# Performance work log

Measured on AMD Instinct MI355X. Metric: run time of the kernel, lower is better.

The kernel has to match this reference:

```python
import jax, jax.numpy as jnp
import numpy as np

N_WIRES = 8
DIM = 2 ** N_WIRES  # 256
NUM_HEADS = 4

def _cnot_ring_perm():
    # Compose CNOT(w, w+1) for w=0..6 then CNOT(7, 0) into one basis permutation.
    # Wire 0 is the most-significant bit of the basis index.
    perm = np.arange(DIM)
    pairs = [(w, w + 1) for w in range(N_WIRES - 1)] + [(N_WIRES - 1, 0)]
    j = np.arange(DIM)
    for c, t in pairs:
        ctrl = (j >> (N_WIRES - 1 - c)) & 1
        M = j ^ (ctrl << (N_WIRES - 1 - t))  # flip target bit where control=1 (involution)
        perm = perm[M]
    return perm

PERM = _cnot_ring_perm()
# SIGNS[i, w] = <i|Z_w|i> = 1 - 2*bit_w(i)
SIGNS = np.array([[1.0 - 2.0 * ((i >> (N_WIRES - 1 - w)) & 1) for w in range(N_WIRES)]
                  for i in range(DIM)], dtype=np.float32)

def setup_inputs() -> dict:
    key = jax.random.key(0)
    k1, k2, k3 = jax.random.split(key, 3)
    x = jax.random.normal(k1, (16, 4096, N_WIRES), jnp.float32)  # rotation angles per token
    theta = jax.random.normal(k2, (N_WIRES,), jnp.float32)       # trainable RX params
    w_combine = jax.random.normal(k3, (N_WIRES, N_WIRES), jnp.float32) / np.float32(np.sqrt(N_WIRES))
    b_combine = jnp.zeros((N_WIRES,), jnp.float32)
    return {"x": x, "theta": theta, "w_combine": w_combine, "b_combine": b_combine}

def _quantum_features(x, theta):
    # RX(x_i) then RX(theta_i) on wire i compose to RX(x_i + theta_i) acting on |0>.
    B, S, E = x.shape
    N = B * S
    phi = (x + theta).reshape(N, E)
    c = jnp.cos(0.5 * phi).astype(jnp.complex64)
    s = (-1j) * jnp.sin(0.5 * phi)          # RX|0> = cos(phi/2)|0> - i sin(phi/2)|1>
    wv = jnp.stack([c, s.astype(jnp.complex64)], axis=-1)  # (N, 8, 2)
    # Build product state via successive Kronecker products (wire 0 = MSB).
    state = jnp.ones((N, 1), jnp.complex64)
    for w in range(E):
        state = (state[:, :, None] * wv[:, w, None, :]).reshape(N, -1)  # (N, 2^(w+1))
    state = state[:, jnp.asarray(PERM)]      # apply the CNOT ring as one permutation
    probs = state.real ** 2 + state.imag ** 2  # (N, 256)
    return (probs @ jnp.asarray(SIGNS)).reshape(B, S, E)  # <Z_w> per token

def reference(x, theta, w_combine, b_combine):
    B, S, E = x.shape
    d_k = E // NUM_HEADS
    q = _quantum_features(x, theta)           # (B, S, 8); k = v = q in the source
    scores = jnp.einsum('bse,bte->bst', q, q) / np.float32(np.sqrt(d_k))
    attn = jax.nn.softmax(scores, axis=-1)    # dropout is identity in eval mode
    out = jnp.einsum('bst,bte->bse', attn, q)
    # Faithful to source: transpose(1,2).contiguous().view(B, S, E)
    out = jnp.swapaxes(out, 1, 2).reshape(B, S, E)
    return out @ w_combine.T + b_combine
```

## Files before the change

### kernel.cpp

```cpp
#include <hip/hip_runtime.h>
#include <math.h>


#define SEQ   4096
#define NB    16
#define SROWS 128
#define TPB   1024
#define NTG   4
#define TC    1024
#define NCH   (SEQ / TC)
#define TILES_PER_TG 8
#define KSTR  12
#define VSTR  1028

typedef _Float16 f16x4  __attribute__((ext_vector_type(4)));
typedef float    f32x16 __attribute__((ext_vector_type(16)));
typedef __fp16   hf2    __attribute__((ext_vector_type(2)));

#if __has_builtin(__builtin_amdgcn_exp2f)
#define EXP2F(x) __builtin_amdgcn_exp2f(x)
#else
#define EXP2F(x) exp2f(x)
#endif

__global__ __launch_bounds__(TPB, 8)
void qattn_kernel(const float* __restrict__ x, const float* __restrict__ theta,
                  const float* __restrict__ wc, const float* __restrict__ bc,
                  float* __restrict__ out)
{
    __shared__ __align__(16) _Float16 kf[TC * KSTR];
    __shared__ __align__(16) _Float16 vt[9 * VSTR];
    float* part = (float*)kf;
    float* attn = (float*)vt;

    const int tid  = threadIdx.x;
    const int lane = tid & 63;
    const int wv   = tid >> 6;
    const int sub  = wv & 3;
    const int tg   = wv >> 2;
    const int l31  = lane & 31;
    const int hp   = lane >> 5;

    const int b  = blockIdx.x >> 5;
    const int S0 = (blockIdx.x & 31) * SROWS;
    const float* xb = x + (size_t)b * SEQ * 8;

    float th[8];
#pragma unroll
    for (int w = 0; w < 8; ++w) th[w] = theta[w];

    vt[8 * VSTR + tid] = (_Float16)1.0f;

    f16x4 qfrag;
    {
        const int s = S0 + sub * 32 + l31;
        const float4 xa  = *(const float4*)(xb + s * 8);
        const float4 xb4 = *(const float4*)(xb + s * 8 + 4);
        float c0 = __cosf(xa.x  + th[0]);
        float c1 = __cosf(xa.y  + th[1]);
        float c2 = __cosf(xa.z  + th[2]);
        float c3 = __cosf(xa.w  + th[3]);
        float c4 = __cosf(xb4.x + th[4]);
        float c5 = __cosf(xb4.y + th[5]);
        float c6 = __cosf(xb4.z + th[6]);
        float c7 = __cosf(xb4.w + th[7]);
        float p1 = c0 * c1, p2 = p1 * c2, p3 = p2 * c3, p4 = p3 * c4;
        float p5 = p4 * c5, p6 = p5 * c6, p7 = p6 * c7;
        float p0 = c1 * c2 * c3 * c4 * c5 * c6 * c7;
        const float sc = 0.70710678118654752f * 1.44269504088896341f;
        if (hp == 0)
            qfrag = (f16x4){(_Float16)(p0*sc), (_Float16)(p1*sc),
                            (_Float16)(p2*sc), (_Float16)(p3*sc)};
        else
            qfrag = (f16x4){(_Float16)(p4*sc), (_Float16)(p5*sc),
                            (_Float16)(p6*sc), (_Float16)(p7*sc)};
    }

    f32x16 o = {0.f,0.f,0.f,0.f,0.f,0.f,0.f,0.f,0.f,0.f,0.f,0.f,0.f,0.f,0.f,0.f};

    const int wr = (l31 < 8) ? l31 : 8;
    const _Float16* kfb = kf + l31 * KSTR + 4 * hp + (tg * TILES_PER_TG) * 32 * KSTR;
    const _Float16* vbb = vt + wr * VSTR + 4 * hp + tg * (TILES_PER_TG * 32);

    float4 pxa = *(const float4*)(xb + tid * 8);
    float4 pxb = *(const float4*)(xb + tid * 8 + 4);

    for (int ch = 0; ch < NCH; ++ch) {
        float c0 = __cosf(pxa.x + th[0]);
        float c1 = __cosf(pxa.y + th[1]);
        float c2 = __cosf(pxa.z + th[2]);
        float c3 = __cosf(pxa.w + th[3]);
        float c4 = __cosf(pxb.x + th[4]);
        float c5 = __cosf(pxb.y + th[5]);
        float c6 = __cosf(pxb.z + th[6]);
        float c7 = __cosf(pxb.w + th[7]);
        float p1 = c0 * c1, p2 = p1 * c2, p3 = p2 * c3, p4 = p3 * c4;
        float p5 = p4 * c5, p6 = p5 * c6, p7 = p6 * c7;
        float p0 = c1 * c2 * c3 * c4 * c5 * c6 * c7;
        _Float16 h0 = (_Float16)p0, h1 = (_Float16)p1, h2 = (_Float16)p2,
                 h3 = (_Float16)p3, h4 = (_Float16)p4, h5 = (_Float16)p5,
                 h6 = (_Float16)p6, h7 = (_Float16)p7;
        __syncthreads();
        {
            _Float16* krow = kf + tid * KSTR;
            *(f16x4*)(krow)     = (f16x4){h0, h1, h2, h3};
            *(f16x4*)(krow + 4) = (f16x4){h4, h5, h6, h7};
            vt[0 * VSTR + tid] = h0;
            vt[1 * VSTR + tid] = h1;
            vt[2 * VSTR + tid] = h2;
            vt[3 * VSTR + tid] = h3;
            vt[4 * VSTR + tid] = h4;
            vt[5 * VSTR + tid] = h5;
            vt[6 * VSTR + tid] = h6;
            vt[7 * VSTR + tid] = h7;
        }
        __syncthreads();
        {
            const int nt = ((ch + 1 < NCH) ? (ch + 1) * TC : ch * TC) + tid;
            pxa = *(const float4*)(xb + nt * 8);
            pxb = *(const float4*)(xb + nt * 8 + 4);
        }
#pragma unroll 4
        for (int i = 0; i < TILES_PER_TG; ++i) {
            f16x4 kfrag = *(const f16x4*)(kfb + i * 32 * KSTR);
            f32x16 cc = __builtin_amdgcn_mfma_f32_32x32x8f16(
                kfrag, qfrag, (f32x16){0.f,0.f,0.f,0.f,0.f,0.f,0.f,0.f,
                                       0.f,0.f,0.f,0.f,0.f,0.f,0.f,0.f}, 0, 0, 0);
#pragma unroll
            for (int u = 0; u < 4; ++u) {
                union { hf2 h[2]; f16x4 v; } pu;
                pu.h[0] = __builtin_amdgcn_cvt_pkrtz(EXP2F(cc[4*u+0]), EXP2F(cc[4*u+1]));
                pu.h[1] = __builtin_amdgcn_cvt_pkrtz(EXP2F(cc[4*u+2]), EXP2F(cc[4*u+3]));
                f16x4 vfrag = *(const f16x4*)(vbb + i * 32 + u * 8);
                o = __builtin_amdgcn_mfma_f32_32x32x8f16(pu.v, vfrag, o, 0, 0, 0);
            }
        }
    }

    __syncthreads();
    if (l31 < 9) {
#pragma unroll
        for (int r = 0; r < 16; ++r) {
            const int sloc = sub * 32 + (r & 3) + 8 * (r >> 2) + 4 * hp;
            part[((tg * SROWS) + sloc) * 9 + l31] = o[r];
        }
    }
    __syncthreads();
    for (int idx = tid; idx < SROWS * 9; idx += TPB) {
        const int rr = idx / 9;
        const int w  = idx - rr * 9;
        float sm = 0.f;
#pragma unroll
        for (int g = 0; g < NTG; ++g) sm += part[((g * SROWS) + rr) * 9 + w];
        attn[rr * 9 + w] = sm;
    }
    __syncthreads();
    if (tid < SROWS * 8) {
        const int rr = tid >> 3;
        const int w  = tid & 7;
        attn[rr * 9 + w] = attn[rr * 9 + w] / attn[rr * 9 + 8];
    }
    __syncthreads();

    if (tid < SROWS) {
        const int e    = tid >> 4;
        const int nloc = tid & 15;
        const int r    = e * 512 + (S0 >> 3) + nloc;
        float y[8];
#pragma unroll
        for (int c = 0; c < 8; ++c) y[c] = attn[(nloc * 8 + c) * 9 + e];
        float oo[8];
#pragma unroll
        for (int k = 0; k < 8; ++k) {
            float a = bc[k];
#pragma unroll
            for (int c = 0; c < 8; ++c) a += y[c] * wc[k * 8 + c];
            oo[k] = a;
        }
        float4* op = (float4*)(out + ((size_t)b * SEQ + r) * 8);
        op[0] = make_float4(oo[0], oo[1], oo[2], oo[3]);
        op[1] = make_float4(oo[4], oo[5], oo[6], oo[7]);
    }
}

extern "C" void kernel_launch(void* const* d_in, const int* in_sizes, int n_in,
                              void* d_out, int out_size, void* d_ws, size_t ws_size,
                              hipStream_t stream)
{
    const float* x  = (const float*)d_in[0];
    const float* th = (const float*)d_in[1];
    const float* wc = (const float*)d_in[2];
    const float* bc = (const float*)d_in[3];
    float* out = (float*)d_out;

    qattn_kernel<<<dim3(NB * (SEQ / SROWS)), dim3(TPB), 0, stream>>>(x, th, wc, bc, out);
}
```

Before: 90.86 us.

## Switch attention MFMAs to 32x32x16 f16 with lane-shuffled P fragments

Replaces the 32x32x8 f16 MFMAs with the gfx950 32x32x16 variant. The score MFMA now runs once per tile with K zero-padded from 8 to 16, and the PV product uses two K=16 MFMAs instead of four K=8 ones, with the exp'd probabilities rearranged across half-waves through xor-32 shuffles. This is meant to halve the matrix instruction count in the inner loop, at the cost of extra cross-lane shuffles, selects and a wider K stride. It also drops the register prefetch of the next chunk's x and loads it inside the barrier region instead, which may expose global load latency.

```diff
diff --git a/kernel.cpp b/kernel.cpp
--- a/kernel.cpp
+++ b/kernel.cpp
@@ -10,10 +10,11 @@
 #define TC    1024
 #define NCH   (SEQ / TC)
 #define TILES_PER_TG 8
-#define KSTR  12
+#define KSTR  20
 #define VSTR  1028
 
 typedef _Float16 f16x4  __attribute__((ext_vector_type(4)));
+typedef _Float16 f16x8  __attribute__((ext_vector_type(8)));
 typedef float    f32x16 __attribute__((ext_vector_type(16)));
 typedef __fp16   hf2    __attribute__((ext_vector_type(2)));
 
@@ -49,9 +50,15 @@
 #pragma unroll
     for (int w = 0; w < 8; ++w) th[w] = theta[w];
 
-    vt[8 * VSTR + tid] = (_Float16)1.0f;
-
-    f16x4 qfrag;
+    {
+        f16x4 z = {(_Float16)0.f, (_Float16)0.f, (_Float16)0.f, (_Float16)0.f};
+        *(f16x4*)(kf + tid * KSTR + 8)  = z;
+        *(f16x4*)(kf + tid * KSTR + 12) = z;
+        vt[8 * VSTR + tid] = (_Float16)1.0f;
+    }
+
+    f16x8 qfrag = {(_Float16)0.f, (_Float16)0.f, (_Float16)0.f, (_Float16)0.f,
+                   (_Float16)0.f, (_Float16)0.f, (_Float16)0.f, (_Float16)0.f};
     {
         const int s = S0 + sub * 32 + l31;
         const float4 xa  = *(const float4*)(xb + s * 8);
@@ -69,39 +76,40 @@
         float p0 = c1 * c2 * c3 * c4 * c5 * c6 * c7;
         const float sc = 0.70710678118654752f * 1.44269504088896341f;
         if (hp == 0)
-            qfrag = (f16x4){(_Float16)(p0*sc), (_Float16)(p1*sc),
-                            (_Float16)(p2*sc), (_Float16)(p3*sc)};
-        else
-            qfrag = (f16x4){(_Float16)(p4*sc), (_Float16)(p5*sc),
+            qfrag = (f16x8){(_Float16)(p0*sc), (_Float16)(p1*sc),
+                            (_Float16)(p2*sc), (_Float16)(p3*sc),
+                            (_Float16)(p4*sc), (_Float16)(p5*sc),
                             (_Float16)(p6*sc), (_Float16)(p7*sc)};
     }
 
-    f32x16 o = {0.f,0.f,0.f,0.f,0.f,0.f,0.f,0.f,0.f,0.f,0.f,0.f,0.f,0.f,0.f,0.f};
+    const f32x16 Z = {0.f,0.f,0.f,0.f,0.f,0.f,0.f,0.f,
+                      0.f,0.f,0.f,0.f,0.f,0.f,0.f,0.f};
+    f32x16 o = Z;
 
     const int wr = (l31 < 8) ? l31 : 8;
-    const _Float16* kfb = kf + l31 * KSTR + 4 * hp + (tg * TILES_PER_TG) * 32 * KSTR;
-    const _Float16* vbb = vt + wr * VSTR + 4 * hp + tg * (TILES_PER_TG * 32);
-
-    float4 pxa = *(const float4*)(xb + tid * 8);
-    float4 pxb = *(const float4*)(xb + tid * 8 + 4);
+    const _Float16* kfb = kf + l31 * KSTR + 8 * hp + (tg * TILES_PER_TG) * 32 * KSTR;
+    const _Float16* vbb = vt + wr * VSTR + 8 * hp + tg * (TILES_PER_TG * 32);
 
     for (int ch = 0; ch < NCH; ++ch) {
-        float c0 = __cosf(pxa.x + th[0]);
-        float c1 = __cosf(pxa.y + th[1]);
-        float c2 = __cosf(pxa.z + th[2]);
-        float c3 = __cosf(pxa.w + th[3]);
-        float c4 = __cosf(pxb.x + th[4]);
-        float c5 = __cosf(pxb.y + th[5]);
-        float c6 = __cosf(pxb.z + th[6]);
-        float c7 = __cosf(pxb.w + th[7]);
-        float p1 = c0 * c1, p2 = p1 * c2, p3 = p2 * c3, p4 = p3 * c4;
-        float p5 = p4 * c5, p6 = p5 * c6, p7 = p6 * c7;
-        float p0 = c1 * c2 * c3 * c4 * c5 * c6 * c7;
-        _Float16 h0 = (_Float16)p0, h1 = (_Float16)p1, h2 = (_Float16)p2,
-                 h3 = (_Float16)p3, h4 = (_Float16)p4, h5 = (_Float16)p5,
-                 h6 = (_Float16)p6, h7 = (_Float16)p7;
         __syncthreads();
         {
+            const int t = ch * TC + tid;
+            const float4 xa  = *(const float4*)(xb + t * 8);
+            const float4 xb4 = *(const float4*)(xb + t * 8 + 4);
+            float c0 = __cosf(xa.x  + th[0]);
+            float c1 = __cosf(xa.y  + th[1]);
+            float c2 = __cosf(xa.z  + th[2]);
+            float c3 = __cosf(xa.w  + th[3]);
+            float c4 = __cosf(xb4.x + th[4]);
+            float c5 = __cosf(xb4.y + th[5]);
+            float c6 = __cosf(xb4.z + th[6]);
+            float c7 = __cosf(xb4.w + th[7]);
+            float p1 = c0 * c1, p2 = p1 * c2, p3 = p2 * c3, p4 = p3 * c4;
+            float p5 = p4 * c5, p6 = p5 * c6, p7 = p6 * c7;
+            float p0 = c1 * c2 * c3 * c4 * c5 * c6 * c7;
+            _Float16 h0 = (_Float16)p0, h1 = (_Float16)p1, h2 = (_Float16)p2,
+                     h3 = (_Float16)p3, h4 = (_Float16)p4, h5 = (_Float16)p5,
+                     h6 = (_Float16)p6, h7 = (_Float16)p7;
             _Float16* krow = kf + tid * KSTR;
             *(f16x4*)(krow)     = (f16x4){h0, h1, h2, h3};
             *(f16x4*)(krow + 4) = (f16x4){h4, h5, h6, h7};
@@ -115,25 +123,45 @@
             vt[7 * VSTR + tid] = h7;
         }
         __syncthreads();
-        {
-            const int nt = ((ch + 1 < NCH) ? (ch + 1) * TC : ch * TC) + tid;
-            pxa = *(const float4*)(xb + nt * 8);
-            pxb = *(const float4*)(xb + nt * 8 + 4);
-        }
-#pragma unroll 4
+#pragma unroll 2
         for (int i = 0; i < TILES_PER_TG; ++i) {
-            f16x4 kfrag = *(const f16x4*)(kfb + i * 32 * KSTR);
-            f32x16 cc = __builtin_amdgcn_mfma_f32_32x32x8f16(
-                kfrag, qfrag, (f32x16){0.f,0.f,0.f,0.f,0.f,0.f,0.f,0.f,
-                                       0.f,0.f,0.f,0.f,0.f,0.f,0.f,0.f}, 0, 0, 0);
-#pragma unroll
-            for (int u = 0; u < 4; ++u) {
-                union { hf2 h[2]; f16x4 v; } pu;
-                pu.h[0] = __builtin_amdgcn_cvt_pkrtz(EXP2F(cc[4*u+0]), EXP2F(cc[4*u+1]));
-                pu.h[1] = __builtin_amdgcn_cvt_pkrtz(EXP2F(cc[4*u+2]), EXP2F(cc[4*u+3]));
-                f16x4 vfrag = *(const f16x4*)(vbb + i * 32 + u * 8);
-                o = __builtin_amdgcn_mfma_f32_32x32x8f16(pu.v, vfrag, o, 0, 0, 0);
+            const _Float16* kp = kfb + i * 32 * KSTR;
+            union { f16x4 h[2]; f16x8 v; } kfr;
+            kfr.h[0] = *(const f16x4*)(kp);
+            kfr.h[1] = *(const f16x4*)(kp + 4);
+            f32x16 cc = __builtin_amdgcn_mfma_f32_32x32x16_f16(kfr.v, qfrag, Z, 0, 0, 0);
+            int ph[8];
+#pragma unroll
+            for (int j = 0; j < 8; ++j) {
+                union { hf2 h; int i_; } t2;
+                t2.h = __builtin_amdgcn_cvt_pkrtz(EXP2F(cc[2*j]), EXP2F(cc[2*j+1]));
+                ph[j] = t2.i_;
             }
+            const int s0 = __shfl_xor(ph[0], 32);
+            const int s1 = __shfl_xor(ph[1], 32);
+            const int s2 = __shfl_xor(ph[2], 32);
+            const int s3 = __shfl_xor(ph[3], 32);
+            const int s4 = __shfl_xor(ph[4], 32);
+            const int s5 = __shfl_xor(ph[5], 32);
+            const int s6 = __shfl_xor(ph[6], 32);
+            const int s7 = __shfl_xor(ph[7], 32);
+            union { int i_[4]; f16x8 v; } A0, A1;
+            A0.i_[0] = hp ? s2    : ph[0];
+            A0.i_[1] = hp ? s3    : ph[1];
+            A0.i_[2] = hp ? ph[2] : s0;
+            A0.i_[3] = hp ? ph[3] : s1;
+            A1.i_[0] = hp ? s6    : ph[4];
+            A1.i_[1] = hp ? s7    : ph[5];
+            A1.i_[2] = hp ? ph[6] : s4;
+            A1.i_[3] = hp ? ph[7] : s5;
+            const _Float16* vp = vbb + i * 32;
+            union { f16x4 h[2]; f16x8 v; } vf0, vf1;
+            vf0.h[0] = *(const f16x4*)(vp);
+            vf0.h[1] = *(const f16x4*)(vp + 4);
+            vf1.h[0] = *(const f16x4*)(vp + 16);
+            vf1.h[1] = *(const f16x4*)(vp + 20);
+            o = __builtin_amdgcn_mfma_f32_32x32x16_f16(A0.v, vf0.v, o, 0, 0, 0);
+            o = __builtin_amdgcn_mfma_f32_32x32x16_f16(A1.v, vf1.v, o, 0, 0, 0);
         }
     }
 
```

Result: slower. 101.4 us (+11.6%).
